# Optimization experiments

Hardware: AMD Instinct MI355X
Metric: run time of the kernel (lower is better)

Reference implementation:

```python
import jax, jax.numpy as jnp
import numpy as np

DIM = 1024
HEADS = 16
HEAD_DIM = DIM // HEADS
HIDDEN = 4 * DIM
EPS = 1e-5


def _layernorm(x, g, b):
    mu = jnp.mean(x, axis=-1, keepdims=True)
    var = jnp.mean(jnp.square(x - mu), axis=-1, keepdims=True)
    return (x - mu) * jax.lax.rsqrt(var + EPS) * g + b


def setup_inputs() -> dict:
    key = jax.random.key(0)
    ks = jax.random.split(key, 10)
    s = lambda fan_in: 1.0 / np.sqrt(fan_in)
    return {
        "x": jax.random.normal(ks[0], (8, 2048, DIM), dtype=jnp.float32),
        # weights stored (in, out): y = x @ W + b
        "w_qkv": jax.random.uniform(ks[1], (DIM, 3 * DIM), minval=-s(DIM), maxval=s(DIM)),
        "b_qkv": jnp.zeros((3 * DIM,), jnp.float32),
        "w_proj": jax.random.uniform(ks[2], (DIM, DIM), minval=-s(DIM), maxval=s(DIM)),
        "b_proj": jnp.zeros((DIM,), jnp.float32),
        "w_fc1": jax.random.uniform(ks[3], (DIM, HIDDEN), minval=-s(DIM), maxval=s(DIM)),
        "b_fc1": jnp.zeros((HIDDEN,), jnp.float32),
        "w_fc2": jax.random.uniform(ks[4], (HIDDEN, DIM), minval=-s(HIDDEN), maxval=s(HIDDEN)),
        "b_fc2": jnp.zeros((DIM,), jnp.float32),
        "g1": jnp.ones((DIM,), jnp.float32),
        "be1": jnp.zeros((DIM,), jnp.float32),
        "g2": jnp.ones((DIM,), jnp.float32),
        "be2": jnp.zeros((DIM,), jnp.float32),
    }


def reference(x, w_qkv, b_qkv, w_proj, b_proj, w_fc1, b_fc1, w_fc2, b_fc2, g1, be1, g2, be2):
    B, N, D = x.shape
    scale = HEAD_DIM ** -0.5

    # --- attention (faithful to source: q,k,v kept as (B,N,H,hd), no head permute) ---
    h = _layernorm(x, g1, be1)
    qkv = (h @ w_qkv + b_qkv).reshape(B, N, 3, HEADS, HEAD_DIM)
    q, k, v = qkv[:, :, 0], qkv[:, :, 1], qkv[:, :, 2]
    # (B,N,H,hd) @ (B,N,hd,H) -> per-token head-head scores (B,N,H,H)
    attn = jnp.einsum('bnhd,bngd->bnhg', q, k) * scale
    attn = jax.nn.softmax(attn, axis=-1)
    o = jnp.einsum('bnhg,bngd->bnhd', attn, v)          # (B,N,H,hd)
    o = jnp.transpose(o, (0, 2, 1, 3)).reshape(B, N, D)  # source's transpose(1,2).reshape
    x = x + o @ w_proj + b_proj

    # --- MLP ---
    h = _layernorm(x, g2, be2)
    h = jax.nn.gelu(h @ w_fc1 + b_fc1, approximate=False)  # torch nn.GELU default = exact
    x = x + h @ w_fc2 + b_fc2
    return x
```

## Files before the change

kernel.cpp:

```cpp
#include <hip/hip_runtime.h>
#include <hip/hip_bf16.h>
#include <math.h>

typedef unsigned short u16;
typedef __attribute__((ext_vector_type(8))) short bf16x8;
typedef __attribute__((ext_vector_type(4))) float f32x4;

#define NTOK 16384
#define SEQ 2048
#define LN_EPS 1e-5f

static __device__ __forceinline__ u16 f2bf(float f) {
  unsigned u = __float_as_uint(f);
  u += 0x7fffu + ((u >> 16) & 1u);
  return (u16)(u >> 16);
}
static __device__ __forceinline__ float bf2f(u16 u) {
  return __uint_as_float(((unsigned)u) << 16);
}

__global__ __launch_bounds__(256) void transpose_bf16(const float* __restrict__ in,
                                                      u16* __restrict__ out,
                                                      int K, int N) {
  __shared__ float tile[32][33];
  int n0 = blockIdx.x * 32, k0 = blockIdx.y * 32;
  int tx = threadIdx.x, ty = threadIdx.y;
#pragma unroll
  for (int i = 0; i < 32; i += 8)
    tile[ty + i][tx] = in[(size_t)(k0 + ty + i) * N + n0 + tx];
  __syncthreads();
#pragma unroll
  for (int i = 0; i < 32; i += 8)
    out[(size_t)(n0 + ty + i) * K + k0 + tx] = f2bf(tile[tx][ty + i]);
}

__global__ __launch_bounds__(256) void ln_bf16(const float* __restrict__ x,
                                               const float* __restrict__ g,
                                               const float* __restrict__ be,
                                               u16* __restrict__ out) {
  __shared__ float red[8];
  int row = blockIdx.x;
  int t = threadIdx.x;
  float4 v = ((const float4*)(x + (size_t)row * 1024))[t];
  float s = v.x + v.y + v.z + v.w;
  float ss = v.x * v.x + v.y * v.y + v.z * v.z + v.w * v.w;
#pragma unroll
  for (int i = 1; i < 64; i <<= 1) {
    s += __shfl_xor(s, i);
    ss += __shfl_xor(ss, i);
  }
  int lane = t & 63, wid = t >> 6;
  if (lane == 0) { red[wid] = s; red[4 + wid] = ss; }
  __syncthreads();
  s = red[0] + red[1] + red[2] + red[3];
  ss = red[4] + red[5] + red[6] + red[7];
  float mu = s * (1.0f / 1024.0f);
  float var = ss * (1.0f / 1024.0f) - mu * mu;
  float rs = rsqrtf(var + LN_EPS);
  float4 gv = ((const float4*)g)[t];
  float4 bv = ((const float4*)be)[t];
  ushort4 o;
  o.x = f2bf((v.x - mu) * rs * gv.x + bv.x);
  o.y = f2bf((v.y - mu) * rs * gv.y + bv.y);
  o.z = f2bf((v.z - mu) * rs * gv.z + bv.z);
  o.w = f2bf((v.w - mu) * rs * gv.w + bv.w);
  ((ushort4*)(out + (size_t)row * 1024))[t] = o;
}

__global__ __launch_bounds__(256) void attn_kernel(const u16* __restrict__ qkv,
                                                   u16* __restrict__ operm) {
  int tok = (blockIdx.x << 2) + (threadIdx.x >> 6);
  int lane = threadIdx.x & 63;
  int h = lane >> 2, sub = lane & 3;
  const u16* base = qkv + (size_t)tok * 3072;
  const u16* qp = base + h * 64;
  const u16* kp = base + 1024;
  const u16* vp = base + 2048;

  float sc[4] = {0.f, 0.f, 0.f, 0.f};
#pragma unroll
  for (int d0 = 0; d0 < 64; d0 += 8) {
    bf16x8 q8 = *(const bf16x8*)(qp + d0);
    float qf[8];
#pragma unroll
    for (int j = 0; j < 8; ++j) qf[j] = bf2f((u16)q8[j]);
#pragma unroll
    for (int gi = 0; gi < 4; ++gi) {
      bf16x8 k8 = *(const bf16x8*)(kp + (sub * 4 + gi) * 64 + d0);
#pragma unroll
      for (int j = 0; j < 8; ++j) sc[gi] += qf[j] * bf2f((u16)k8[j]);
    }
  }
  const float scale = 0.125f;
#pragma unroll
  for (int gi = 0; gi < 4; ++gi) sc[gi] *= scale;
  float mx = fmaxf(fmaxf(sc[0], sc[1]), fmaxf(sc[2], sc[3]));
  mx = fmaxf(mx, __shfl_xor(mx, 1));
  mx = fmaxf(mx, __shfl_xor(mx, 2));
  float p[4], sum = 0.f;
#pragma unroll
  for (int gi = 0; gi < 4; ++gi) { p[gi] = expf(sc[gi] - mx); sum += p[gi]; }
  sum += __shfl_xor(sum, 1);
  sum += __shfl_xor(sum, 2);
  float inv = 1.0f / sum;
#pragma unroll
  for (int gi = 0; gi < 4; ++gi) p[gi] *= inv;

  float pall[16];
#pragma unroll
  for (int g = 0; g < 16; ++g)
    pall[g] = __shfl(p[g & 3], (lane & ~3) | (g >> 2));

  float o[16];
#pragma unroll
  for (int j = 0; j < 16; ++j) o[j] = 0.f;
#pragma unroll
  for (int g = 0; g < 16; ++g) {
    bf16x8 v0 = *(const bf16x8*)(vp + g * 64 + sub * 16);
    bf16x8 v1 = *(const bf16x8*)(vp + g * 64 + sub * 16 + 8);
#pragma unroll
    for (int j = 0; j < 8; ++j) {
      o[j] += pall[g] * bf2f((u16)v0[j]);
      o[8 + j] += pall[g] * bf2f((u16)v1[j]);
    }
  }
  int b = tok >> 11, n = tok & 2047;
  size_t off = ((size_t)b << 21) + (size_t)(h * 128 + (n >> 4)) * 1024 +
               (size_t)((n & 15) * 64 + sub * 16);
  bf16x8 w0, w1;
#pragma unroll
  for (int j = 0; j < 8; ++j) {
    w0[j] = (short)f2bf(o[j]);
    w1[j] = (short)f2bf(o[8 + j]);
  }
  *(bf16x8*)(operm + off) = w0;
  *(bf16x8*)(operm + off + 8) = w1;
}

template <int EPI>
__global__ __launch_bounds__(256) void gemm_bt(const u16* __restrict__ A,
                                               const u16* __restrict__ BT,
                                               const float* __restrict__ bias,
                                               const float* __restrict__ res,
                                               void* __restrict__ outp,
                                               int M, int N, int K) {
  __shared__ u16 As[128 * 64];
  __shared__ u16 Bs[128 * 64];
  const int tid = threadIdx.x;
  const int wid = tid >> 6, lane = tid & 63;
  const int wm = wid >> 1, wn = wid & 1;
  const int bn = blockIdx.x, bm = blockIdx.y;
  const int lrow = lane & 15, lhi = lane >> 4;

  const size_t a_tile = (size_t)bm * 128 * K;
  const size_t b_tile = (size_t)bn * 128 * K;

  int lds_off[4];
  size_t g_off[4];
#pragma unroll
  for (int i = 0; i < 4; ++i) {
    int c = wid * 4 + i;
    int s = c * 64 + lane;
    int row = s >> 3;
    int k8 = (s & 7) ^ (row & 7);
    lds_off[i] = c * 512;
    g_off[i] = (size_t)row * K + (size_t)(k8 * 8);
  }

  f32x4 acc[4][4] = {};

  const int nkt = K >> 6;
  for (int kt = 0; kt < nkt; ++kt) {
    const size_t koff = (size_t)kt * 64;
#pragma unroll
    for (int i = 0; i < 4; ++i) {
      __builtin_amdgcn_global_load_lds(
          (const __attribute__((address_space(1))) void*)(A + a_tile + koff + g_off[i]),
          (__attribute__((address_space(3))) void*)(As + lds_off[i]), 16, 0, 0);
      __builtin_amdgcn_global_load_lds(
          (const __attribute__((address_space(1))) void*)(BT + b_tile + koff + g_off[i]),
          (__attribute__((address_space(3))) void*)(Bs + lds_off[i]), 16, 0, 0);
    }
    __syncthreads();
#pragma unroll
    for (int t2 = 0; t2 < 2; ++t2) {
      bf16x8 af[4], bfv[4];
      const int k8 = t2 * 4 + lhi;
#pragma unroll
      for (int m = 0; m < 4; ++m) {
        int row = wm * 64 + m * 16 + lrow;
        af[m] = *(const bf16x8*)(As + row * 64 + ((k8 ^ (row & 7)) << 3));
      }
#pragma unroll
      for (int n = 0; n < 4; ++n) {
        int row = wn * 64 + n * 16 + lrow;
        bfv[n] = *(const bf16x8*)(Bs + row * 64 + ((k8 ^ (row & 7)) << 3));
      }
#pragma unroll
      for (int m = 0; m < 4; ++m)
#pragma unroll
        for (int n = 0; n < 4; ++n)
          acc[m][n] = __builtin_amdgcn_mfma_f32_16x16x32_bf16(af[m], bfv[n], acc[m][n], 0, 0, 0);
    }
    __syncthreads();
  }

  const size_t crow0 = (size_t)bm * 128 + wm * 64;
  const int ccol0 = bn * 128 + wn * 64;
#pragma unroll
  for (int n = 0; n < 4; ++n) {
    int col = ccol0 + n * 16 + lrow;
    float bb = bias[col];
#pragma unroll
    for (int m = 0; m < 4; ++m) {
#pragma unroll
      for (int r = 0; r < 4; ++r) {
        size_t row = crow0 + m * 16 + lhi * 4 + r;
        size_t idx = row * (size_t)N + col;
        float val = acc[m][n][r] + bb;
        if (EPI == 1 || EPI == 3) val += res[idx];
        if (EPI == 2) val = 0.5f * val * (1.0f + erff(val * 0.70710678118654752f));
        if (EPI == 0 || EPI == 2)
          ((u16*)outp)[idx] = f2bf(val);
        else
          ((float*)outp)[idx] = val;
      }
    }
  }
}

extern "C" void kernel_launch(void* const* d_in, const int* in_sizes, int n_in,
                              void* d_out, int out_size, void* d_ws, size_t ws_size,
                              hipStream_t stream) {
  const float* x = (const float*)d_in[0];
  const float* w_qkv = (const float*)d_in[1];
  const float* b_qkv = (const float*)d_in[2];
  const float* w_proj = (const float*)d_in[3];
  const float* b_proj = (const float*)d_in[4];
  const float* w_fc1 = (const float*)d_in[5];
  const float* b_fc1 = (const float*)d_in[6];
  const float* w_fc2 = (const float*)d_in[7];
  const float* b_fc2 = (const float*)d_in[8];
  const float* g1 = (const float*)d_in[9];
  const float* be1 = (const float*)d_in[10];
  const float* g2 = (const float*)d_in[11];
  const float* be2 = (const float*)d_in[12];
  float* out = (float*)d_out;

  char* ws = (char*)d_ws;
  u16* wqkvT = (u16*)ws; ws += (size_t)3072 * 1024 * 2;
  u16* wprojT = (u16*)ws; ws += (size_t)1024 * 1024 * 2;
  u16* wfc1T = (u16*)ws; ws += (size_t)4096 * 1024 * 2;
  u16* wfc2T = (u16*)ws; ws += (size_t)1024 * 4096 * 2;
  u16* hbuf = (u16*)ws; ws += (size_t)NTOK * 1024 * 2;
  u16* big = (u16*)ws;

  transpose_bf16<<<dim3(3072 / 32, 1024 / 32), dim3(32, 8), 0, stream>>>(w_qkv, wqkvT, 1024, 3072);
  transpose_bf16<<<dim3(1024 / 32, 1024 / 32), dim3(32, 8), 0, stream>>>(w_proj, wprojT, 1024, 1024);
  transpose_bf16<<<dim3(4096 / 32, 1024 / 32), dim3(32, 8), 0, stream>>>(w_fc1, wfc1T, 1024, 4096);
  transpose_bf16<<<dim3(1024 / 32, 4096 / 32), dim3(32, 8), 0, stream>>>(w_fc2, wfc2T, 4096, 1024);

  ln_bf16<<<NTOK, 256, 0, stream>>>(x, g1, be1, hbuf);

  gemm_bt<0><<<dim3(3072 / 128, NTOK / 128), 256, 0, stream>>>(hbuf, wqkvT, b_qkv, nullptr, big, NTOK, 3072, 1024);

  attn_kernel<<<NTOK / 4, 256, 0, stream>>>(big, hbuf);

  gemm_bt<1><<<dim3(1024 / 128, NTOK / 128), 256, 0, stream>>>(hbuf, wprojT, b_proj, x, out, NTOK, 1024, 1024);

  ln_bf16<<<NTOK, 256, 0, stream>>>(out, g2, be2, hbuf);

  gemm_bt<2><<<dim3(4096 / 128, NTOK / 128), 256, 0, stream>>>(hbuf, wfc1T, b_fc1, nullptr, big, NTOK, 4096, 1024);

  gemm_bt<3><<<dim3(1024 / 128, NTOK / 128), 256, 0, stream>>>(big, wfc2T, b_fc2, out, out, NTOK, 1024, 4096);
}
```

Baseline: 733.2 us.

## Replace GEMM with 256x256 double-buffered pipelined kernel with block swizzle

Replaces the 128x128 single-buffered GEMM with a 256x256 tile, 512-thread kernel. It double-buffers LDS and interleaves the direct-to-LDS global loads for the next tiles between MFMA groups, using explicit vmcnt waits, barriers and setprio. It also swizzles workgroup order to improve L2 reuse. The goal is to overlap memory with compute and raise arithmetic intensity per block, at the cost of heavy register pressure (128 accumulator floats) and 128KB of LDS per block.

```diff
diff --git a/kernel.cpp b/kernel.cpp
--- a/kernel.cpp
+++ b/kernel.cpp
@@ -7,7 +7,6 @@
 typedef __attribute__((ext_vector_type(4))) float f32x4;
 
 #define NTOK 16384
-#define SEQ 2048
 #define LN_EPS 1e-5f
 
 static __device__ __forceinline__ u16 f2bf(float f) {
@@ -138,85 +137,137 @@
 }
 
 template <int EPI>
-__global__ __launch_bounds__(256) void gemm_bt(const u16* __restrict__ A,
-                                               const u16* __restrict__ BT,
-                                               const float* __restrict__ bias,
-                                               const float* __restrict__ res,
-                                               void* __restrict__ outp,
-                                               int M, int N, int K) {
-  __shared__ u16 As[128 * 64];
-  __shared__ u16 Bs[128 * 64];
+__global__ __launch_bounds__(512, 2) void gemm256(const u16* __restrict__ A,
+                                                  const u16* __restrict__ BT,
+                                                  const float* __restrict__ bias,
+                                                  const float* __restrict__ res,
+                                                  void* __restrict__ outp,
+                                                  int M, int N, int K) {
+  __shared__ u16 As[2][256 * 64];
+  __shared__ u16 Bs[2][256 * 64];
   const int tid = threadIdx.x;
   const int wid = tid >> 6, lane = tid & 63;
-  const int wm = wid >> 1, wn = wid & 1;
-  const int bn = blockIdx.x, bm = blockIdx.y;
+  const int wm = wid >> 2, wn = wid & 3;
   const int lrow = lane & 15, lhi = lane >> 4;
 
-  const size_t a_tile = (size_t)bm * 128 * K;
-  const size_t b_tile = (size_t)bn * 128 * K;
-
-  int lds_off[4];
-  size_t g_off[4];
-#pragma unroll
-  for (int i = 0; i < 4; ++i) {
-    int c = wid * 4 + i;
-    int s = c * 64 + lane;
-    int row = s >> 3;
-    int k8 = (s & 7) ^ (row & 7);
-    lds_off[i] = c * 512;
-    g_off[i] = (size_t)row * K + (size_t)(k8 * 8);
-  }
-
-  f32x4 acc[4][4] = {};
-
-  const int nkt = K >> 6;
-  for (int kt = 0; kt < nkt; ++kt) {
-    const size_t koff = (size_t)kt * 64;
-#pragma unroll
-    for (int i = 0; i < 4; ++i) {
+  const int nbx = gridDim.x;
+  const int nwg = nbx * gridDim.y;
+  const int wg = blockIdx.y * nbx + blockIdx.x;
+  const int cpx = nwg >> 3;
+  const int swz = (wg & 7) * cpx + (wg >> 3);
+  const int bn = swz % nbx, bm = swz / nbx;
+
+  const int NT = K >> 6;
+
+  const int r8 = tid >> 3;
+  const int k8s = (tid & 7) ^ (r8 & 7);
+  const u16* pA = A + (size_t)(bm * 256 + r8) * K + k8s * 8;
+  const u16* pB = BT + (size_t)(bn * 256 + r8) * K + k8s * 8;
+  const int ldsbase = wid * 512;
+
+  auto stage2 = [&](int t, int pair) {
+    if (t >= NT) return;
+    const u16* g = (pair < 2 ? pA : pB) + (size_t)t * 64;
+    u16* l = (pair < 2 ? &As[t & 1][0] : &Bs[t & 1][0]);
+#pragma unroll
+    for (int j = 0; j < 2; ++j) {
+      const int i = (pair & 1) * 2 + j;
       __builtin_amdgcn_global_load_lds(
-          (const __attribute__((address_space(1))) void*)(A + a_tile + koff + g_off[i]),
-          (__attribute__((address_space(3))) void*)(As + lds_off[i]), 16, 0, 0);
-      __builtin_amdgcn_global_load_lds(
-          (const __attribute__((address_space(1))) void*)(BT + b_tile + koff + g_off[i]),
-          (__attribute__((address_space(3))) void*)(Bs + lds_off[i]), 16, 0, 0);
-    }
-    __syncthreads();
-#pragma unroll
-    for (int t2 = 0; t2 < 2; ++t2) {
-      bf16x8 af[4], bfv[4];
-      const int k8 = t2 * 4 + lhi;
-#pragma unroll
-      for (int m = 0; m < 4; ++m) {
-        int row = wm * 64 + m * 16 + lrow;
-        af[m] = *(const bf16x8*)(As + row * 64 + ((k8 ^ (row & 7)) << 3));
-      }
+          (const __attribute__((address_space(1))) void*)(g + (size_t)i * 64 * K),
+          (__attribute__((address_space(3))) void*)(l + i * 4096 + ldsbase), 16, 0, 0);
+    }
+  };
+
+  stage2(0, 0); stage2(0, 1); stage2(0, 2); stage2(0, 3);
+  stage2(1, 0); stage2(1, 1); stage2(1, 2);
+
+  f32x4 acc[8][4] = {};
+  const int rbA = wm * 128 + lrow;
+  const int rbB = wn * 64 + lrow;
+  const int sl0 = ((0 + lhi) ^ (lrow & 7)) << 3;
+  const int sl1 = ((4 + lhi) ^ (lrow & 7)) << 3;
+
+  for (int t = 0; t < NT; ++t) {
+    if (t == NT - 1) {
+      asm volatile("s_waitcnt vmcnt(0)" ::: "memory");
+    } else {
+      asm volatile("s_waitcnt vmcnt(6)" ::: "memory");
+    }
+    stage2(t + 1, 3);
+    __builtin_amdgcn_s_barrier();
+    __builtin_amdgcn_sched_barrier(0);
+
+    const u16* Ab = &As[t & 1][0];
+    const u16* Bb = &Bs[t & 1][0];
+    bf16x8 af[8][2], bf[4][2];
+#pragma unroll
+    for (int n = 0; n < 4; ++n) {
+      bf[n][0] = *(const bf16x8*)(Bb + (rbB + n * 16) * 64 + sl0);
+      bf[n][1] = *(const bf16x8*)(Bb + (rbB + n * 16) * 64 + sl1);
+    }
+#pragma unroll
+    for (int m = 0; m < 8; ++m) {
+      af[m][0] = *(const bf16x8*)(Ab + (rbA + m * 16) * 64 + sl0);
+      af[m][1] = *(const bf16x8*)(Ab + (rbA + m * 16) * 64 + sl1);
+    }
+    __builtin_amdgcn_s_setprio(1);
+#pragma unroll
+    for (int mm = 0; mm < 2; ++mm)
 #pragma unroll
       for (int n = 0; n < 4; ++n) {
-        int row = wn * 64 + n * 16 + lrow;
-        bfv[n] = *(const bf16x8*)(Bs + row * 64 + ((k8 ^ (row & 7)) << 3));
-      }
-#pragma unroll
-      for (int m = 0; m < 4; ++m)
-#pragma unroll
-        for (int n = 0; n < 4; ++n)
-          acc[m][n] = __builtin_amdgcn_mfma_f32_16x16x32_bf16(af[m], bfv[n], acc[m][n], 0, 0, 0);
-    }
-    __syncthreads();
-  }
-
-  const size_t crow0 = (size_t)bm * 128 + wm * 64;
-  const int ccol0 = bn * 128 + wn * 64;
+        acc[mm][n] = __builtin_amdgcn_mfma_f32_16x16x32_bf16(af[mm][0], bf[n][0], acc[mm][n], 0, 0, 0);
+        acc[mm][n] = __builtin_amdgcn_mfma_f32_16x16x32_bf16(af[mm][1], bf[n][1], acc[mm][n], 0, 0, 0);
+      }
+    __builtin_amdgcn_s_setprio(0);
+
+    asm volatile("s_waitcnt lgkmcnt(0)" ::: "memory");
+    __builtin_amdgcn_s_barrier();
+    __builtin_amdgcn_sched_barrier(0);
+
+    stage2(t + 2, 0);
+    __builtin_amdgcn_s_setprio(1);
+#pragma unroll
+    for (int mm = 2; mm < 4; ++mm)
+#pragma unroll
+      for (int n = 0; n < 4; ++n) {
+        acc[mm][n] = __builtin_amdgcn_mfma_f32_16x16x32_bf16(af[mm][0], bf[n][0], acc[mm][n], 0, 0, 0);
+        acc[mm][n] = __builtin_amdgcn_mfma_f32_16x16x32_bf16(af[mm][1], bf[n][1], acc[mm][n], 0, 0, 0);
+      }
+    __builtin_amdgcn_s_setprio(0);
+    stage2(t + 2, 1);
+    __builtin_amdgcn_s_setprio(1);
+#pragma unroll
+    for (int mm = 4; mm < 6; ++mm)
+#pragma unroll
+      for (int n = 0; n < 4; ++n) {
+        acc[mm][n] = __builtin_amdgcn_mfma_f32_16x16x32_bf16(af[mm][0], bf[n][0], acc[mm][n], 0, 0, 0);
+        acc[mm][n] = __builtin_amdgcn_mfma_f32_16x16x32_bf16(af[mm][1], bf[n][1], acc[mm][n], 0, 0, 0);
+      }
+    __builtin_amdgcn_s_setprio(0);
+    stage2(t + 2, 2);
+    __builtin_amdgcn_s_setprio(1);
+#pragma unroll
+    for (int mm = 6; mm < 8; ++mm)
+#pragma unroll
+      for (int n = 0; n < 4; ++n) {
+        acc[mm][n] = __builtin_amdgcn_mfma_f32_16x16x32_bf16(af[mm][0], bf[n][0], acc[mm][n], 0, 0, 0);
+        acc[mm][n] = __builtin_amdgcn_mfma_f32_16x16x32_bf16(af[mm][1], bf[n][1], acc[mm][n], 0, 0, 0);
+      }
+    __builtin_amdgcn_s_setprio(0);
+  }
+
+  const size_t crow0 = (size_t)bm * 256 + (size_t)wm * 128;
+  const int ccol0 = bn * 256 + wn * 64;
 #pragma unroll
   for (int n = 0; n < 4; ++n) {
-    int col = ccol0 + n * 16 + lrow;
-    float bb = bias[col];
-#pragma unroll
-    for (int m = 0; m < 4; ++m) {
+    const int col = ccol0 + n * 16 + lrow;
+    const float bb = bias[col];
+#pragma unroll
+    for (int m = 0; m < 8; ++m) {
 #pragma unroll
       for (int r = 0; r < 4; ++r) {
-        size_t row = crow0 + m * 16 + lhi * 4 + r;
-        size_t idx = row * (size_t)N + col;
+        const size_t row = crow0 + m * 16 + lhi * 4 + r;
+        const size_t idx = row * (size_t)N + col;
         float val = acc[m][n][r] + bb;
         if (EPI == 1 || EPI == 3) val += res[idx];
         if (EPI == 2) val = 0.5f * val * (1.0f + erff(val * 0.70710678118654752f));
@@ -262,15 +313,15 @@
 
   ln_bf16<<<NTOK, 256, 0, stream>>>(x, g1, be1, hbuf);
 
-  gemm_bt<0><<<dim3(3072 / 128, NTOK / 128), 256, 0, stream>>>(hbuf, wqkvT, b_qkv, nullptr, big, NTOK, 3072, 1024);
+  gemm256<0><<<dim3(3072 / 256, NTOK / 256), 512, 0, stream>>>(hbuf, wqkvT, b_qkv, nullptr, big, NTOK, 3072, 1024);
 
   attn_kernel<<<NTOK / 4, 256, 0, stream>>>(big, hbuf);
 
-  gemm_bt<1><<<dim3(1024 / 128, NTOK / 128), 256, 0, stream>>>(hbuf, wprojT, b_proj, x, out, NTOK, 1024, 1024);
+  gemm256<1><<<dim3(1024 / 256, NTOK / 256), 512, 0, stream>>>(hbuf, wprojT, b_proj, x, out, NTOK, 1024, 1024);
 
   ln_bf16<<<NTOK, 256, 0, stream>>>(out, g2, be2, hbuf);
 
-  gemm_bt<2><<<dim3(4096 / 128, NTOK / 128), 256, 0, stream>>>(hbuf, wfc1T, b_fc1, nullptr, big, NTOK, 4096, 1024);
-
-  gemm_bt<3><<<dim3(1024 / 128, NTOK / 128), 256, 0, stream>>>(big, wfc2T, b_fc2, out, out, NTOK, 1024, 4096);
-}
+  gemm256<2><<<dim3(4096 / 256, NTOK / 256), 512, 0, stream>>>(hbuf, wfc1T, b_fc1, nullptr, big, NTOK, 4096, 1024);
+
+  gemm256<3><<<dim3(1024 / 256, NTOK / 256), 512, 0, stream>>>(big, wfc2T, b_fc2, out, out, NTOK, 1024, 4096);
+}
```

Measured after the change: 674.5 us. 1.09x faster.
